# Kernel tuning notes

Measured on AMD Instinct MI355X. Metric: run time of the kernel, lower is better.

## Reference

```python
import jax, jax.numpy as jnp
import numpy as np

B, N = 8, 2048
DIN, DS, DO, GE, HID = 2, 32, 32, 8, 32
CHEB_K = 3
N_SUPPORTS = 2
D_CAT = DIN + 2 * DS            # 66, input to the two AGCNs
D_BASIS = N_SUPPORTS * CHEB_K * D_CAT  # 396


def setup_inputs() -> dict:
    key = jax.random.key(0)
    ks = jax.random.split(key, 12)
    xt = jax.random.normal(ks[0], (B, N, DIN), dtype=jnp.float32)
    state1 = jax.random.normal(ks[1], (B, N, DS), dtype=jnp.float32)
    state2 = jax.random.normal(ks[2], (B, N, DS), dtype=jnp.float32)
    gatembedding = jax.random.normal(ks[3], (B, N, GE), dtype=jnp.float32)
    # adaptive adjacency supports: row-stochastic (softmax over neighbors), 2 supports
    supports = jax.nn.softmax(jax.random.normal(ks[4], (N_SUPPORTS, B, N, N), dtype=jnp.float32), axis=-1)

    def xavier(k, shape):
        fan_in, fan_out = shape[0], shape[1]
        std = float(np.sqrt(2.0 / (fan_in + fan_out)))
        return jax.random.normal(k, shape, dtype=jnp.float32) * std

    return {
        "xt": xt, "state1": state1, "state2": state2,
        "gatembedding": gatembedding, "supports": supports,
        "mlp_w": xavier(ks[5], (DIN + 2 * DS + GE, DO)), "mlp_b": jnp.zeros((DO,), jnp.float32),
        "gate_w": xavier(ks[6], (D_BASIS, 3 * DO)), "gate_b": jnp.zeros((3 * DO,), jnp.float32),
        "upd_w": xavier(ks[7], (D_BASIS, DO)), "upd_b": jnp.zeros((DO,), jnp.float32),
        "hop_w": xavier(ks[8], (DO, HID)), "hop_b": jnp.zeros((HID,), jnp.float32),
    }


def _agcn(x, supports, W, b):
    """Chebyshev graph conv: for each support, basis T0=I, T1=A, Tk=2A Tk-1 - Tk-2,
    applied to x (linearity lets us recurse on T_k @ x directly, same math)."""
    terms = []
    for i in range(N_SUPPORTS):  # fixed small structural loop
        A = supports[i]                                  # [B,N,N]
        t_prev, t_cur = x, jnp.einsum('bnm,bmc->bnc', A, x)
        ts = [t_prev, t_cur]
        for _ in range(2, CHEB_K):
            t_prev, t_cur = t_cur, 2.0 * jnp.einsum('bnm,bmc->bnc', A, t_cur) - t_prev
            ts.append(t_cur)
        terms.extend(ts)
    x_g = jnp.concatenate(terms, axis=-1)                # [B,N,2*K*c]
    return jnp.einsum('bni,io->bno', x_g, W) + b


def reference(xt, state1, state2, gatembedding, supports,
              mlp_w, mlp_b, gate_w, gate_b, upd_w, upd_b, hop_w, hop_b):
    # MLP mixing gate between the two incoming states
    gate_in = jnp.concatenate([xt, state1, state2, gatembedding], axis=-1)
    mr = jax.nn.sigmoid(gate_in @ mlp_w + mlp_b)
    state = mr * state1 + (1.0 - mr) * state2
    # graph-conv GRU gates
    X = jnp.concatenate([xt, state1, state2], axis=-1)   # [B,N,DIN+2*DS]
    zz_r = jax.nn.sigmoid(_agcn(X, supports, gate_w, gate_b))
    z1, z2, r = zz_r[..., :DO], zz_r[..., DO:2 * DO], zz_r[..., 2 * DO:]
    candidate = jnp.concatenate([xt, z1 * state1, z2 * state2], axis=-1)
    hc = jnp.tanh(_agcn(candidate, supports, upd_w, upd_b))
    h = r * state + (1.0 - r) * hc                        # [B,N,DO]
    transnext = h @ hop_w + hop_b                         # [B,N,HID]
    return (h, transnext)
```

## Files before the change

kernel.cpp:

```cpp
#include <hip/hip_runtime.h>

#define NN 2048
#define BB 8
#define KT 416
#define SLOT (80 * NN)

typedef __bf16 bf16;
typedef __bf16 bf16x4 __attribute__((ext_vector_type(4)));
typedef __bf16 bf16x8 __attribute__((ext_vector_type(8)));
typedef float  f32x4  __attribute__((ext_vector_type(4)));

__device__ __forceinline__ void bar_lgkm() {
    asm volatile("s_waitcnt lgkmcnt(0)" ::: "memory");
    __builtin_amdgcn_s_barrier();
}

__global__ void prep_weights(const float* __restrict__ gw, const float* __restrict__ uw,
                             bf16* __restrict__ Wg, bf16* __restrict__ Wu)
{
    int i = blockIdx.x * 256 + threadIdx.x;
    if (i < 96 * KT) {
        int o = i / KT, k = i % KT, t = k / 80, c = k % 80;
        float v = 0.0f;
        if (c < 66) {
            if (t == 0)      v = gw[c*96+o] - gw[(132+c)*96+o] + gw[(198+c)*96+o] - gw[(330+c)*96+o];
            else if (t == 1) v = gw[(66+c)*96+o];
            else if (t == 2) v = 2.0f * gw[(132+c)*96+o];
            else if (t == 3) v = gw[(264+c)*96+o];
            else             v = 2.0f * gw[(330+c)*96+o];
        }
        Wg[i] = (bf16)v;
    }
    if (i < 32 * KT) {
        int o = i / KT, k = i % KT, t = k / 80, c = k % 80;
        float v = 0.0f;
        if (c < 66) {
            if (t == 0)      v = uw[c*32+o] - uw[(132+c)*32+o] + uw[(198+c)*32+o] - uw[(330+c)*32+o];
            else if (t == 1) v = uw[(66+c)*32+o];
            else if (t == 2) v = 2.0f * uw[(132+c)*32+o];
            else if (t == 3) v = uw[(264+c)*32+o];
            else             v = 2.0f * uw[(330+c)*32+o];
        }
        Wu[i] = (bf16)v;
    }
}

__global__ __launch_bounds__(256)
void prep_nodes(const float* __restrict__ xt, const float* __restrict__ s1,
                const float* __restrict__ s2, const float* __restrict__ ge,
                const float* __restrict__ mlp_w, const float* __restrict__ mlp_b,
                float* __restrict__ state, bf16* __restrict__ T)
{
    __shared__ float wl[74 * 32];
    __shared__ float bl[32];
    __shared__ __align__(16) float statel[64][36];
    __shared__ __align__(16) bf16  Xl[80][72];
    const int tid = threadIdx.x;

    for (int i = tid; i < 592; i += 256) ((float4*)wl)[i] = ((const float4*)mlp_w)[i];
    if (tid < 32) bl[tid] = mlp_b[tid];
    {
        int bb = blockIdx.x >> 5, chunk = blockIdx.x & 31;
        uint2* dst = (uint2*)((char*)T + ((size_t)bb * KT * NN + 400 * NN) * 2 + (size_t)chunk * 2048);
        dst[tid] = make_uint2(0u, 0u);
    }
    for (int i = tid; i < 14 * 64; i += 256) Xl[66 + (i >> 6)][i & 63] = (bf16)0.0f;
    __syncthreads();

    const int nl = tid & 63, og = tid >> 6, o0 = og * 8;
    const size_t node0 = (size_t)blockIdx.x * 64;
    const size_t node = node0 + nl;
    const int b = (int)(node0 >> 11);
    const int nb0 = (int)(node0 & 2047);
    const float* p1 = s1 + node * 32;
    const float* p2 = s2 + node * 32;
    const float* pg = ge + node * 8;

    float acc[8];
    #pragma unroll
    for (int j = 0; j < 8; ++j) acc[j] = bl[o0 + j];
    float2 px = *(const float2*)(xt + node * 2);
    #pragma unroll
    for (int j = 0; j < 8; ++j) acc[j] += px.x * wl[o0 + j] + px.y * wl[32 + o0 + j];

    float k1[8], k2[8];
    #pragma unroll
    for (int ii = 0; ii < 8; ++ii) {
        float4 v = *(const float4*)(p1 + ii * 4);
        const float* vp = (const float*)&v;
        if (ii == 2 * og)     { k1[0]=vp[0]; k1[1]=vp[1]; k1[2]=vp[2]; k1[3]=vp[3]; }
        if (ii == 2 * og + 1) { k1[4]=vp[0]; k1[5]=vp[1]; k1[6]=vp[2]; k1[7]=vp[3]; }
        #pragma unroll
        for (int p = 0; p < 4; ++p) {
            #pragma unroll
            for (int j = 0; j < 8; ++j) acc[j] += vp[p] * wl[(2 + ii*4 + p) * 32 + o0 + j];
        }
    }
    #pragma unroll
    for (int ii = 0; ii < 8; ++ii) {
        float4 v = *(const float4*)(p2 + ii * 4);
        const float* vp = (const float*)&v;
        if (ii == 2 * og)     { k2[0]=vp[0]; k2[1]=vp[1]; k2[2]=vp[2]; k2[3]=vp[3]; }
        if (ii == 2 * og + 1) { k2[4]=vp[0]; k2[5]=vp[1]; k2[6]=vp[2]; k2[7]=vp[3]; }
        #pragma unroll
        for (int p = 0; p < 4; ++p) {
            #pragma unroll
            for (int j = 0; j < 8; ++j) acc[j] += vp[p] * wl[(34 + ii*4 + p) * 32 + o0 + j];
        }
    }
    #pragma unroll
    for (int ii = 0; ii < 2; ++ii) {
        float4 v = *(const float4*)(pg + ii * 4);
        const float* vp = (const float*)&v;
        #pragma unroll
        for (int p = 0; p < 4; ++p) {
            #pragma unroll
            for (int j = 0; j < 8; ++j) acc[j] += vp[p] * wl[(66 + ii*4 + p) * 32 + o0 + j];
        }
    }
    #pragma unroll
    for (int j = 0; j < 8; ++j) {
        float mr = 1.0f / (1.0f + __expf(-acc[j]));
        statel[nl][o0 + j] = mr * k1[j] + (1.0f - mr) * k2[j];
        Xl[2 + o0 + j][nl]  = (bf16)k1[j];
        Xl[34 + o0 + j][nl] = (bf16)k2[j];
    }
    if (og == 0) { Xl[0][nl] = (bf16)px.x; Xl[1][nl] = (bf16)px.y; }
    __syncthreads();

    for (int i = tid; i < 512; i += 256) {
        int n_ = i >> 3, c = (i & 7) * 4;
        *(float4*)&state[node0 * 32 + n_ * 32 + c] = *(const float4*)&statel[n_][c];
    }
    bf16* Tb = T + (size_t)b * KT * NN;
    for (int i = tid; i < 640; i += 256) {
        int r = i >> 3, seg = i & 7;
        *(uint4*)(Tb + (size_t)r * NN + nb0 + seg * 8) = *(const uint4*)&Xl[r][seg * 8];
    }
}

template<int MODE>
__global__ __launch_bounds__(256, 2)
void gemm_cheb(const float* __restrict__ Aall, bf16* Abf, bf16* T,
               int in0, int in1, int out0, int out1)
{
    __shared__ __align__(16) bf16 lB[2][2][80][40];

    const int sb = blockIdx.y;
    const int s = sb >> 3, b = sb & 7;
    const int m0 = blockIdx.x * 64;
    const float* A = Aall + (size_t)sb * NN * NN + (size_t)m0 * NN;
    bf16* Ab = Abf + (size_t)sb * NN * NN + (size_t)m0 * NN;
    bf16* Tb = T + (size_t)b * KT * NN;
    const bf16* Bt = Tb + (size_t)(s ? in1 : in0) * SLOT;
    bf16*       Ct = Tb + (size_t)(s ? out1 : out0) * SLOT + m0;

    const int tid  = threadIdx.x;
    const int wave = tid >> 6;
    const int lane = tid & 63;
    const int frow = lane & 15;
    const int fko  = (lane >> 4) * 8;
    const int am   = wave * 16 + frow;

    const float* Af = A  + (size_t)am * NN + fko;
    const bf16*  Ap = Ab + (size_t)am * NN + fko;
    bf16*        As = Ab + (size_t)am * NN + fko;

    const int brow  = tid >> 2, bseg = tid & 3;
    const int brow2 = 64 + (tid >> 2);

    auto gloadB = [&](uint4& r0h0, uint4& r1h0, uint4& r0h1, uint4& r1h1, int k0) {
        r0h0 = *(const uint4*)(Bt + (size_t)brow * NN + k0 + bseg * 8);
        r0h1 = *(const uint4*)(Bt + (size_t)brow * NN + k0 + 32 + bseg * 8);
        if (tid < 64) {
            r1h0 = *(const uint4*)(Bt + (size_t)brow2 * NN + k0 + bseg * 8);
            r1h1 = *(const uint4*)(Bt + (size_t)brow2 * NN + k0 + 32 + bseg * 8);
        }
    };
    auto stageB = [&](int buf, uint4& r0h0, uint4& r1h0, uint4& r0h1, uint4& r1h1) {
        *(uint4*)&lB[buf][0][brow][bseg * 8] = r0h0;
        *(uint4*)&lB[buf][1][brow][bseg * 8] = r0h1;
        if (tid < 64) {
            *(uint4*)&lB[buf][0][brow2][bseg * 8] = r1h0;
            *(uint4*)&lB[buf][1][brow2][bseg * 8] = r1h1;
        }
    };
    auto gloadA = [&](uint4& h0, uint4& h1, float4& g00, float4& g01,
                      float4& g10, float4& g11, int k0) {
        if constexpr (MODE == 2) {
            h0 = *(const uint4*)(Ap + k0);
            h1 = *(const uint4*)(Ap + k0 + 32);
        } else {
            g00 = *(const float4*)(Af + k0);
            g01 = *(const float4*)(Af + k0 + 4);
            g10 = *(const float4*)(Af + k0 + 32);
            g11 = *(const float4*)(Af + k0 + 36);
        }
    };
    auto mkaf = [&](uint4& h, float4& g0, float4& g1, int k0) -> bf16x8 {
        if constexpr (MODE == 2) {
            return *(bf16x8*)&h;
        } else {
            bf16x8 r;
            r[0]=(bf16)g0.x; r[1]=(bf16)g0.y; r[2]=(bf16)g0.z; r[3]=(bf16)g0.w;
            r[4]=(bf16)g1.x; r[5]=(bf16)g1.y; r[6]=(bf16)g1.z; r[7]=(bf16)g1.w;
            if constexpr (MODE == 1) *(bf16x8*)(As + k0) = r;
            return r;
        }
    };

    f32x4 acc[5] = {};
    auto compute = [&](int buf, bf16x8 af0, bf16x8 af1) {
        #pragma unroll
        for (int ct = 0; ct < 5; ++ct) {
            bf16x8 bv = *(const bf16x8*)&lB[buf][0][ct * 16 + frow][fko];
            acc[ct] = __builtin_amdgcn_mfma_f32_16x16x32_bf16(af0, bv, acc[ct], 0, 0, 0);
        }
        #pragma unroll
        for (int ct = 0; ct < 5; ++ct) {
            bf16x8 bv = *(const bf16x8*)&lB[buf][1][ct * 16 + frow][fko];
            acc[ct] = __builtin_amdgcn_mfma_f32_16x16x32_bf16(af1, bv, acc[ct], 0, 0, 0);
        }
    };

    uint4 b00A, b10A, b01A, b11A, b00B, b10B, b01B, b11B;
    uint4 a0A, a1A, a0B, a1B;
    float4 f00A, f01A, f10A, f11A, f00B, f01B, f10B, f11B;

    gloadB(b00A, b10A, b01A, b11A, 0);
    gloadB(b00B, b10B, b01B, b11B, 64);
    gloadA(a0A, a1A, f00A, f01A, f10A, f11A, 0);
    gloadA(a0B, a1B, f00B, f01B, f10B, f11B, 64);

    for (int it = 0; it < 32; it += 2) {
        stageB(0, b00A, b10A, b01A, b11A);
        bf16x8 e0 = mkaf(a0A, f00A, f01A, it * 64);
        bf16x8 e1 = mkaf(a1A, f10A, f11A, it * 64 + 32);
        if (it < 30) {
            gloadB(b00A, b10A, b01A, b11A, (it + 2) * 64);
            gloadA(a0A, a1A, f00A, f01A, f10A, f11A, (it + 2) * 64);
        }
        bar_lgkm();
        compute(0, e0, e1);
        stageB(1, b00B, b10B, b01B, b11B);
        bf16x8 o0 = mkaf(a0B, f00B, f01B, (it + 1) * 64);
        bf16x8 o1 = mkaf(a1B, f10B, f11B, (it + 1) * 64 + 32);
        if (it < 29) {
            gloadB(b00B, b10B, b01B, b11B, (it + 3) * 64);
            gloadA(a0B, a1B, f00B, f01B, f10B, f11B, (it + 3) * 64);
        }
        bar_lgkm();
        compute(1, o0, o1);
    }

    const int ccol = lane & 15;
    const int crow = (lane >> 4) * 4;
    #pragma unroll
    for (int ct = 0; ct < 5; ++ct) {
        bf16x4 o;
        o[0]=(bf16)acc[ct][0]; o[1]=(bf16)acc[ct][1]; o[2]=(bf16)acc[ct][2]; o[3]=(bf16)acc[ct][3];
        *(bf16x4*)&Ct[(size_t)(ct * 16 + ccol) * NN + wave * 16 + crow] = o;
    }
}

__global__ __launch_bounds__(256)
void proj_gate(const bf16* T, const bf16* __restrict__ Wg, const float* __restrict__ gate_b,
               const float* __restrict__ s1, const float* __restrict__ s2,
               bf16* Tmut, float* __restrict__ rT)
{
    __shared__ __align__(16) bf16 Wl[96][424];
    __shared__ __align__(16) bf16 Bl[2][64][44];
    const int b = blockIdx.y, n0 = blockIdx.x * 64, tid = threadIdx.x;
    const bf16* Tb = T + (size_t)b * KT * NN;

    for (int i = tid; i < 96 * 52; i += 256) {
        int r = i / 52, seg = i % 52;
        *(uint4*)&Wl[r][seg * 8] = *(const uint4*)(Wg + (size_t)r * KT + seg * 8);
    }
    const int kk = tid >> 3, seg = tid & 7;
    uint4 rbA, rbB;
    auto gloadv = [&](uint4& r, int k0) { r = *(const uint4*)(Tb + (size_t)(k0 + kk) * NN + n0 + seg * 8); };
    auto scat = [&](int buf, uint4& r) {
        bf16 tmp[8]; *(uint4*)tmp = r;
        #pragma unroll
        for (int j = 0; j < 8; ++j) Bl[buf][seg * 8 + j][kk] = tmp[j];
    };
    const int lane = tid & 63, wave = tid >> 6;
    const int fr = lane & 15, qd = lane >> 4;

    f32x4 acc[6] = {};
    auto comp = [&](int buf, int st) {
        bf16x8 bv = *(const bf16x8*)&Bl[buf][wave * 16 + fr][qd * 8];
        #pragma unroll
        for (int f = 0; f < 6; ++f) {
            bf16x8 av = *(const bf16x8*)&Wl[f * 16 + fr][st * 32 + qd * 8];
            acc[f] = __builtin_amdgcn_mfma_f32_16x16x32_bf16(av, bv, acc[f], 0, 0, 0);
        }
    };

    gloadv(rbA, 0); gloadv(rbB, 32);
    for (int st = 0; st < 12; st += 2) {
        scat(0, rbA);
        gloadv(rbA, (st + 2) * 32);
        bar_lgkm();
        comp(0, st);
        scat(1, rbB);
        if (st < 10) gloadv(rbB, (st + 3) * 32);
        bar_lgkm();
        comp(1, st + 1);
    }
    scat(0, rbA);
    bar_lgkm();
    comp(0, 12);

    const int nn = n0 + wave * 16 + fr;
    const size_t node = (size_t)b * NN + nn;
    bf16* Cd = Tmut + (size_t)b * KT * NN;
    #pragma unroll
    for (int f = 0; f < 6; ++f) {
        const int o0 = f * 16 + qd * 4;
        float4 gb4 = *(const float4*)(gate_b + o0);
        const float* gb = (const float*)&gb4;
        float sg[4];
        #pragma unroll
        for (int r = 0; r < 4; ++r) sg[r] = 1.0f / (1.0f + __expf(-(acc[f][r] + gb[r])));
        if (f < 2) {
            float4 sv4 = *(const float4*)(s1 + node * 32 + o0);
            const float* sv = (const float*)&sv4;
            #pragma unroll
            for (int r = 0; r < 4; ++r) Cd[(size_t)(2 + o0 + r) * NN + nn] = (bf16)(sg[r] * sv[r]);
        } else if (f < 4) {
            const int oo = o0 - 32;
            float4 sv4 = *(const float4*)(s2 + node * 32 + oo);
            const float* sv = (const float*)&sv4;
            #pragma unroll
            for (int r = 0; r < 4; ++r) Cd[(size_t)(34 + oo + r) * NN + nn] = (bf16)(sg[r] * sv[r]);
        } else {
            const int oo = o0 - 64;
            #pragma unroll
            for (int r = 0; r < 4; ++r) rT[((size_t)b * 32 + oo + r) * NN + nn] = sg[r];
        }
    }
}

__global__ __launch_bounds__(256)
void proj_upd(const bf16* __restrict__ T, const bf16* __restrict__ Wu,
              const float* __restrict__ upd_b, const float* __restrict__ state,
              const float* __restrict__ rT, const float* __restrict__ hop_w,
              const float* __restrict__ hop_b, float* __restrict__ out)
{
    __shared__ __align__(16) bf16 Wl[32][424];
    __shared__ __align__(16) bf16 Bl[2][64][44];
    __shared__ __align__(16) float hsh[64][36];
    __shared__ float hw[1024];
    const int b = blockIdx.y, n0 = blockIdx.x * 64, tid = threadIdx.x;
    const bf16* Tb = T + (size_t)b * KT * NN;

    for (int i = tid; i < 32 * 52; i += 256) {
        int r = i / 52, seg = i % 52;
        *(uint4*)&Wl[r][seg * 8] = *(const uint4*)(Wu + (size_t)r * KT + seg * 8);
    }
    for (int i = tid; i < 256; i += 256) ((float4*)hw)[i] = ((const float4*)hop_w)[i];
    const int kk = tid >> 3, seg = tid & 7;
    uint4 rbA, rbB;
    auto gloadv = [&](uint4& r, int k0) { r = *(const uint4*)(Tb + (size_t)(k0 + kk) * NN + n0 + seg * 8); };
    auto scat = [&](int buf, uint4& r) {
        bf16 tmp[8]; *(uint4*)tmp = r;
        #pragma unroll
        for (int j = 0; j < 8; ++j) Bl[buf][seg * 8 + j][kk] = tmp[j];
    };
    const int lane = tid & 63, wave = tid >> 6;
    const int fr = lane & 15, qd = lane >> 4;

    f32x4 acc[2] = {};
    auto comp = [&](int buf, int st) {
        bf16x8 bv = *(const bf16x8*)&Bl[buf][wave * 16 + fr][qd * 8];
        #pragma unroll
        for (int f = 0; f < 2; ++f) {
            bf16x8 av = *(const bf16x8*)&Wl[f * 16 + fr][st * 32 + qd * 8];
            acc[f] = __builtin_amdgcn_mfma_f32_16x16x32_bf16(av, bv, acc[f], 0, 0, 0);
        }
    };

    gloadv(rbA, 0); gloadv(rbB, 32);
    for (int st = 0; st < 12; st += 2) {
        scat(0, rbA);
        gloadv(rbA, (st + 2) * 32);
        bar_lgkm();
        comp(0, st);
        scat(1, rbB);
        if (st < 10) gloadv(rbB, (st + 3) * 32);
        bar_lgkm();
        comp(1, st + 1);
    }
    scat(0, rbA);
    bar_lgkm();
    comp(0, 12);

    const int nn = n0 + wave * 16 + fr;
    const size_t node = (size_t)b * NN + nn;
    const int nl = wave * 16 + fr;
    #pragma unroll
    for (int f = 0; f < 2; ++f) {
        const int o0 = f * 16 + qd * 4;
        float4 ub4 = *(const float4*)(upd_b + o0);
        const float* ub = (const float*)&ub4;
        float4 st4 = *(const float4*)(state + node * 32 + o0);
        const float* sv = (const float*)&st4;
        #pragma unroll
        for (int r = 0; r < 4; ++r) {
            const int o = o0 + r;
            float hc = tanhf(acc[f][r] + ub[r]);
            float rv = rT[((size_t)b * 32 + o) * NN + nn];
            hsh[nl][o] = rv * sv[r] + (1.0f - rv) * hc;
        }
    }
    __syncthreads();

    const int nl2 = tid & 63, og = tid >> 6;
    const size_t node2 = (size_t)b * NN + n0 + nl2;
    float tac[8];
    #pragma unroll
    for (int j = 0; j < 8; ++j) tac[j] = hop_b[og * 8 + j];
    #pragma unroll
    for (int kc = 0; kc < 8; ++kc) {
        float4 hv4 = *(const float4*)&hsh[nl2][kc * 4];
        const float* hv = (const float*)&hv4;
        #pragma unroll
        for (int p = 0; p < 4; ++p) {
            #pragma unroll
            for (int j = 0; j < 8; ++j) tac[j] += hv[p] * hw[(kc * 4 + p) * 32 + og * 8 + j];
        }
    }
    float* out2 = out + (size_t)BB * NN * 32;
    *(float4*)&out[node2 * 32 + og * 8]     = *(const float4*)&hsh[nl2][og * 8];
    *(float4*)&out[node2 * 32 + og * 8 + 4] = *(const float4*)&hsh[nl2][og * 8 + 4];
    float4 t0; float* t0p = (float*)&t0;
    t0p[0]=tac[0]; t0p[1]=tac[1]; t0p[2]=tac[2]; t0p[3]=tac[3];
    *(float4*)&out2[node2 * 32 + og * 8] = t0;
    t0p[0]=tac[4]; t0p[1]=tac[5]; t0p[2]=tac[6]; t0p[3]=tac[7];
    *(float4*)&out2[node2 * 32 + og * 8 + 4] = t0;
}

extern "C" void kernel_launch(void* const* d_in, const int* in_sizes, int n_in,
                              void* d_out, int out_size, void* d_ws, size_t ws_size,
                              hipStream_t stream)
{
    const float* xt     = (const float*)d_in[0];
    const float* s1     = (const float*)d_in[1];
    const float* s2     = (const float*)d_in[2];
    const float* ge     = (const float*)d_in[3];
    const float* sup    = (const float*)d_in[4];
    const float* mlp_w  = (const float*)d_in[5];
    const float* mlp_b  = (const float*)d_in[6];
    const float* gate_w = (const float*)d_in[7];
    const float* gate_b = (const float*)d_in[8];
    const float* upd_w  = (const float*)d_in[9];
    const float* upd_b  = (const float*)d_in[10];
    const float* hop_w  = (const float*)d_in[11];
    const float* hop_b  = (const float*)d_in[12];
    float* out = (float*)d_out;

    char* ws = (char*)d_ws;
    size_t off = 0;
    auto alloc = [&](size_t bytes) -> void* {
        void* p = ws + off;
        off += (bytes + 255) & ~(size_t)255;
        return p;
    };
    bf16*  T     = (bf16*) alloc((size_t)BB * KT * NN * 2);
    float* state = (float*)alloc((size_t)BB * NN * 32 * 4);
    float* rT    = (float*)alloc((size_t)BB * 32 * NN * 4);
    bf16*  Wg    = (bf16*) alloc((size_t)96 * KT * 2);
    bf16*  Wu    = (bf16*) alloc((size_t)32 * KT * 2);
    bf16*  Abf   = (bf16*) (ws + off);
    const bool useA = (off + (size_t)16 * NN * NN * 2) <= ws_size;

    prep_weights<<<156, 256, 0, stream>>>(gate_w, upd_w, Wg, Wu);
    prep_nodes<<<256, 256, 0, stream>>>(xt, s1, s2, ge, mlp_w, mlp_b, state, T);

    if (useA) {
        gemm_cheb<1><<<dim3(32, 16), 256, 0, stream>>>(sup, Abf, T, 0, 0, 1, 3);
        gemm_cheb<2><<<dim3(32, 16), 256, 0, stream>>>(sup, Abf, T, 1, 3, 2, 4);
        proj_gate<<<dim3(32, 8), 256, 0, stream>>>(T, Wg, gate_b, s1, s2, T, rT);
        gemm_cheb<2><<<dim3(32, 16), 256, 0, stream>>>(sup, Abf, T, 0, 0, 1, 3);
        gemm_cheb<2><<<dim3(32, 16), 256, 0, stream>>>(sup, Abf, T, 1, 3, 2, 4);
    } else {
        gemm_cheb<0><<<dim3(32, 16), 256, 0, stream>>>(sup, Abf, T, 0, 0, 1, 3);
        gemm_cheb<0><<<dim3(32, 16), 256, 0, stream>>>(sup, Abf, T, 1, 3, 2, 4);
        proj_gate<<<dim3(32, 8), 256, 0, stream>>>(T, Wg, gate_b, s1, s2, T, rT);
        gemm_cheb<0><<<dim3(32, 16), 256, 0, stream>>>(sup, Abf, T, 0, 0, 1, 3);
        gemm_cheb<0><<<dim3(32, 16), 256, 0, stream>>>(sup, Abf, T, 1, 3, 2, 4);
    }
    proj_upd<<<dim3(32, 8), 256, 0, stream>>>(T, Wu, upd_b, state, rT, hop_w, hop_b, out);
}
```

Baseline: 548.7 us.

## Fuse paired Chebyshev GEMM launches with a software grid barrier

```diff
diff --git a/kernel.cpp b/kernel.cpp
--- a/kernel.cpp
+++ b/kernel.cpp
@@ -15,10 +15,32 @@
     __builtin_amdgcn_s_barrier();
 }
 
+__device__ __forceinline__ void gsync(unsigned* bar, unsigned nb) {
+    __syncthreads();
+    if (threadIdx.x == 0) {
+        __threadfence();
+        unsigned g = __hip_atomic_load(&bar[1], __ATOMIC_RELAXED, __HIP_MEMORY_SCOPE_AGENT);
+        unsigned a = __hip_atomic_fetch_add(&bar[0], 1u, __ATOMIC_ACQ_REL, __HIP_MEMORY_SCOPE_AGENT);
+        if (a == nb - 1) {
+            __hip_atomic_store(&bar[0], 0u, __ATOMIC_RELAXED, __HIP_MEMORY_SCOPE_AGENT);
+            __hip_atomic_store(&bar[1], g + 1u, __ATOMIC_RELEASE, __HIP_MEMORY_SCOPE_AGENT);
+        } else {
+            for (int i = 0; i < (1 << 20); ++i) {
+                if (__hip_atomic_load(&bar[1], __ATOMIC_ACQUIRE, __HIP_MEMORY_SCOPE_AGENT) != g) break;
+                __builtin_amdgcn_s_sleep(8);
+            }
+        }
+        __threadfence();
+    }
+    __syncthreads();
+}
+
 __global__ void prep_weights(const float* __restrict__ gw, const float* __restrict__ uw,
-                             bf16* __restrict__ Wg, bf16* __restrict__ Wu)
+                             bf16* __restrict__ Wg, bf16* __restrict__ Wu,
+                             unsigned* __restrict__ bar)
 {
     int i = blockIdx.x * 256 + threadIdx.x;
+    if (i < 2) bar[i] = 0u;
     if (i < 96 * KT) {
         int o = i / KT, k = i % KT, t = k / 80, c = k % 80;
         float v = 0.0f;
@@ -140,12 +162,11 @@
 }
 
 template<int MODE>
-__global__ __launch_bounds__(256, 2)
-void gemm_cheb(const float* __restrict__ Aall, bf16* Abf, bf16* T,
-               int in0, int in1, int out0, int out1)
-{
-    __shared__ __align__(16) bf16 lB[2][2][80][40];
-
+__device__ __forceinline__ void gemm_body(
+    const float* __restrict__ Aall, bf16* __restrict__ Abf, bf16* __restrict__ T,
+    int in0, int in1, int out0, int out1,
+    bf16 (&lB)[2][2][80][40])
+{
     const int sb = blockIdx.y;
     const int s = sb >> 3, b = sb & 7;
     const int m0 = blockIdx.x * 64;
@@ -261,6 +282,17 @@
         o[0]=(bf16)acc[ct][0]; o[1]=(bf16)acc[ct][1]; o[2]=(bf16)acc[ct][2]; o[3]=(bf16)acc[ct][3];
         *(bf16x4*)&Ct[(size_t)(ct * 16 + ccol) * NN + wave * 16 + crow] = o;
     }
+}
+
+template<int M0, int M1>
+__global__ __launch_bounds__(256, 2)
+void gemm_fused(const float* __restrict__ Aall, bf16* Abf, bf16* T,
+                unsigned* __restrict__ bar)
+{
+    __shared__ __align__(16) bf16 lB[2][2][80][40];
+    gemm_body<M0>(Aall, Abf, T, 0, 0, 1, 3, lB);
+    gsync(bar, gridDim.x * gridDim.y);
+    gemm_body<M1>(Aall, Abf, T, 1, 3, 2, 4, lB);
 }
 
 __global__ __launch_bounds__(256)
@@ -473,24 +505,21 @@
     float* rT    = (float*)alloc((size_t)BB * 32 * NN * 4);
     bf16*  Wg    = (bf16*) alloc((size_t)96 * KT * 2);
     bf16*  Wu    = (bf16*) alloc((size_t)32 * KT * 2);
+    unsigned* bar = (unsigned*)alloc(256);
     bf16*  Abf   = (bf16*) (ws + off);
     const bool useA = (off + (size_t)16 * NN * NN * 2) <= ws_size;
 
-    prep_weights<<<156, 256, 0, stream>>>(gate_w, upd_w, Wg, Wu);
+    prep_weights<<<156, 256, 0, stream>>>(gate_w, upd_w, Wg, Wu, bar);
     prep_nodes<<<256, 256, 0, stream>>>(xt, s1, s2, ge, mlp_w, mlp_b, state, T);
 
     if (useA) {
-        gemm_cheb<1><<<dim3(32, 16), 256, 0, stream>>>(sup, Abf, T, 0, 0, 1, 3);
-        gemm_cheb<2><<<dim3(32, 16), 256, 0, stream>>>(sup, Abf, T, 1, 3, 2, 4);
+        gemm_fused<1, 2><<<dim3(32, 16), 256, 0, stream>>>(sup, Abf, T, bar);
         proj_gate<<<dim3(32, 8), 256, 0, stream>>>(T, Wg, gate_b, s1, s2, T, rT);
-        gemm_cheb<2><<<dim3(32, 16), 256, 0, stream>>>(sup, Abf, T, 0, 0, 1, 3);
-        gemm_cheb<2><<<dim3(32, 16), 256, 0, stream>>>(sup, Abf, T, 1, 3, 2, 4);
+        gemm_fused<2, 2><<<dim3(32, 16), 256, 0, stream>>>(sup, Abf, T, bar);
     } else {
-        gemm_cheb<0><<<dim3(32, 16), 256, 0, stream>>>(sup, Abf, T, 0, 0, 1, 3);
-        gemm_cheb<0><<<dim3(32, 16), 256, 0, stream>>>(sup, Abf, T, 1, 3, 2, 4);
+        gemm_fused<0, 0><<<dim3(32, 16), 256, 0, stream>>>(sup, Abf, T, bar);
         proj_gate<<<dim3(32, 8), 256, 0, stream>>>(T, Wg, gate_b, s1, s2, T, rT);
-        gemm_cheb<0><<<dim3(32, 16), 256, 0, stream>>>(sup, Abf, T, 0, 0, 1, 3);
-        gemm_cheb<0><<<dim3(32, 16), 256, 0, stream>>>(sup, Abf, T, 1, 3, 2, 4);
+        gemm_fused<0, 0><<<dim3(32, 16), 256, 0, stream>>>(sup, Abf, T, bar);
     }
     proj_upd<<<dim3(32, 8), 256, 0, stream>>>(T, Wu, upd_b, state, rT, hop_w, hop_b, out);
 }
```

Measured after the change: 746.9 us. +36.1%, slower.
